# Kernel tuning notes

Measured on AMD Instinct MI355X. Metric: run time of the kernel, lower is better.

Reference implementation:

```python
import jax, jax.numpy as jnp
import numpy as np

C = 320        # in_channels == inner_dim (n_heads*d_head = 8*40)
HEADS = 8
DH = 40
CTX = 768
FF_INNER = 1280  # 4*C
G = 32         # GroupNorm groups


def _ln(x, w, b, eps=1e-5):
    m = x.mean(-1, keepdims=True)
    v = ((x - m) ** 2).mean(-1, keepdims=True)
    return (x - m) * jax.lax.rsqrt(v + eps) * w + b


def _attn(q, k, v, heads, scale):
    # faithful to source: split last dim as (d h) -> head index is fastest
    B, Lq, D = q.shape
    Lk = k.shape[1]
    dh = D // heads
    q = q.reshape(B, Lq, dh, heads).transpose(0, 3, 1, 2)  # b h i d
    k = k.reshape(B, Lk, dh, heads).transpose(0, 3, 1, 2)  # b h j d
    v = v.reshape(B, Lk, dh, heads).transpose(0, 3, 1, 2)
    sim = jnp.einsum('bhid,bhjd->bhij', q, k) * scale
    w = jax.nn.softmax(sim, axis=-1)
    o = jnp.einsum('bhij,bhjd->bhid', w, v)
    # merge as (h d): head index is slowest on output (matches source)
    return o.transpose(0, 2, 1, 3).reshape(B, Lq, heads * dh)


def setup_inputs() -> dict:
    key = jax.random.key(0)
    ks = jax.random.split(key, 20)
    n = lambda i, shape: jax.random.normal(ks[i], shape, jnp.float32) * 0.02
    z = lambda d: jnp.zeros((d,), jnp.float32)
    o = lambda d: jnp.ones((d,), jnp.float32)
    return dict(
        x=jax.random.normal(ks[0], (1, C, 64, 64), jnp.float32),
        context=jax.random.normal(ks[1], (1, 77, CTX), jnp.float32),
        gn_w=o(C), gn_b=z(C),
        w_in=n(2, (C, C)), b_in=z(C),
        ln1_w=o(C), ln1_b=z(C),
        wq1=n(3, (C, C)), wk1=n(4, (C, C)), wv1=n(5, (C, C)),
        wo1=n(6, (C, C)), bo1=z(C),
        ln2_w=o(C), ln2_b=z(C),
        wq2=n(7, (C, C)), wk2=n(8, (CTX, C)), wv2=n(9, (CTX, C)),
        wo2=n(10, (C, C)), bo2=z(C),
        ln3_w=o(C), ln3_b=z(C),
        wff1=n(11, (C, 2 * FF_INNER)), bff1=z(2 * FF_INNER),
        wff2=n(12, (FF_INNER, C)), bff2=z(C),
        w_out=n(13, (C, C)), b_out=z(C),
    )


def reference(x, context, gn_w, gn_b, w_in, b_in,
              ln1_w, ln1_b, wq1, wk1, wv1, wo1, bo1,
              ln2_w, ln2_b, wq2, wk2, wv2, wo2, bo2,
              ln3_w, ln3_b, wff1, bff1, wff2, bff2,
              w_out, b_out):
    B, Cc, H, W = x.shape
    scale = DH ** (-0.5)
    x_in = x
    # GroupNorm(32, eps=1e-6)
    g = x.reshape(B, G, Cc // G, H, W)
    m = g.mean((2, 3, 4), keepdims=True)
    v = ((g - m) ** 2).mean((2, 3, 4), keepdims=True)
    h = ((g - m) * jax.lax.rsqrt(v + 1e-6)).reshape(B, Cc, H, W)
    h = h * gn_w[None, :, None, None] + gn_b[None, :, None, None]
    # 1x1 conv in_proj
    h = jnp.einsum('bchw,co->bohw', h, w_in) + b_in[None, :, None, None]
    # b c h w -> b (h w) c
    t = h.transpose(0, 2, 3, 1).reshape(B, H * W, C)
    # --- transformer block (depth=1) ---
    # attn_1: self-attn; NOTE source applies k/v proj to the QUERY projection
    hn = _ln(t, ln1_w, ln1_b)
    q = hn @ wq1
    k = q @ wk1
    vv = q @ wv1
    t = t + (_attn(q, k, vv, HEADS, scale) @ wo1 + bo1)
    # attn_2: cross-attn with context
    hn = _ln(t, ln2_w, ln2_b)
    q = hn @ wq2
    k = context @ wk2
    vv = context @ wv2
    t = t + (_attn(q, k, vv, HEADS, scale) @ wo2 + bo2)
    # GEGLU feed-forward
    hn = _ln(t, ln3_w, ln3_b)
    p = hn @ wff1 + bff1
    a, gate = p[..., :FF_INNER], p[..., FF_INNER:]
    t = t + ((a * jax.nn.gelu(gate, approximate=False)) @ wff2 + bff2)
    # b (h w) c -> b c h w
    s = t.reshape(B, H, W, C).transpose(0, 3, 1, 2)
    out = jnp.einsum('bchw,co->bohw', s, w_out) + b_out[None, :, None, None]
    return out + x_in
```

## Files before the change

kernel.cpp:

```cpp
#include <hip/hip_runtime.h>
#include <hip/hip_bf16.h>
#include <math.h>

#define CCH 320
#define NHEADS 8
#define DH 40
#define HW 4096
#define FFI 1280

typedef __bf16 bf16x8 __attribute__((ext_vector_type(8)));
typedef unsigned short u16x8 __attribute__((ext_vector_type(8)));
typedef short s16x4 __attribute__((ext_vector_type(4)));
typedef float f32x4 __attribute__((ext_vector_type(4)));
typedef unsigned int u32x4 __attribute__((ext_vector_type(4)));

__device__ inline unsigned short f2bf(float f) {
    __hip_bfloat16 h = __float2bfloat16(f);
    return __builtin_bit_cast(unsigned short, h);
}
__device__ inline unsigned pk2bf(float a, float b) {
#if __has_builtin(__builtin_amdgcn_cvt_pk_bf16_f32)
    typedef __bf16 bf16x2 __attribute__((ext_vector_type(2)));
    bf16x2 r = __builtin_amdgcn_cvt_pk_bf16_f32(a, b);
    return __builtin_bit_cast(unsigned, r);
#else
    return (unsigned)f2bf(a) | ((unsigned)f2bf(b) << 16);
#endif
}
__device__ inline float bf2f(unsigned short u) {
    return __builtin_bit_cast(float, ((unsigned)u) << 16);
}
__device__ inline bf16x8 ldfrag(const unsigned short* p) {
    u16x8 raw = *reinterpret_cast<const u16x8*>(p);
    return __builtin_bit_cast(bf16x8, raw);
}
__device__ inline s16x4 pk2frag(unsigned a, unsigned b) {
    unsigned long long v = (unsigned long long)a | ((unsigned long long)b << 32);
    return __builtin_bit_cast(s16x4, v);
}

__global__ __launch_bounds__(256) void prep_w2(
    const float* __restrict__ w_in, const float* __restrict__ wq1,
    const float* __restrict__ wk1, const float* __restrict__ wv1,
    const float* __restrict__ wo1, const float* __restrict__ wq2,
    const float* __restrict__ wo2, const float* __restrict__ w_out,
    const float* __restrict__ wff1, const float* __restrict__ wff2,
    const float* __restrict__ wk2, const float* __restrict__ wv2,
    unsigned short* __restrict__ Wt) {
    __shared__ float tile[64][65];
    const int b = blockIdx.x, tid = threadIdx.x;
    const float* src;
    int K, stride, dstoff, k0, n0;
    bool glu = false;
    if (b < 200) {
        int m = b / 25, t = b % 25;
        k0 = (t / 5) * 64; n0 = (t % 5) * 64;
        K = 320; stride = 320; dstoff = m * 102400;
        src = (m == 0) ? w_in : (m == 1) ? wq1 : (m == 2) ? wk1 :
              (m == 3) ? wv1 : (m == 4) ? wo1 : (m == 5) ? wq2 :
              (m == 6) ? wo2 : w_out;
    } else if (b < 300) {
        int t = b - 200;
        k0 = (t / 5) * 64; n0 = (t % 5) * 64;
        K = 1280; stride = 320; dstoff = 1638400; src = wff2;
    } else if (b < 500) {
        int t = b - 300;
        k0 = (t / 40) * 64; n0 = (t % 40) * 64;
        K = 320; stride = 2560; dstoff = 819200; src = wff1; glu = true;
    } else if (b < 560) {
        int t = b - 500;
        k0 = (t / 5) * 64; n0 = (t % 5) * 64;
        K = 768; stride = 320; dstoff = 2048000; src = wk2;
    } else {
        int t = b - 560;
        k0 = (t / 5) * 64; n0 = (t % 5) * 64;
        K = 768; stride = 320; dstoff = 2048000 + 245760; src = wv2;
    }
#pragma unroll
    for (int i = 0; i < 16; ++i) {
        int idx = tid + i * 256;
        int r = idx >> 6, cn = idx & 63;
        int scol = glu ? ((n0 >> 1) + (cn >> 1) + (cn & 1) * FFI) : (n0 + cn);
        tile[r][cn] = src[(size_t)(k0 + r) * stride + scol];
    }
    __syncthreads();
#pragma unroll
    for (int i = 0; i < 16; ++i) {
        int idx = tid + i * 256;
        int cl = idx >> 6, cr = idx & 63;
        Wt[dstoff + (size_t)(n0 + cl) * K + k0 + cr] = f2bf(tile[cr][cl]);
    }
}

__global__ void pack_ctx(const float* __restrict__ ctx,
                         unsigned short* __restrict__ D) {
    int idx = blockIdx.x * 256 + threadIdx.x;
    int row = idx / 768, col = idx - row * 768;
    float v = (row < 77) ? ctx[row * 768 + col] : 0.f;
    D[idx] = f2bf(v);
}

__global__ __launch_bounds__(256) void gn_stats(const float* __restrict__ X,
                                                float2* __restrict__ part) {
    __shared__ float s1[256], s2[256];
    const int b = blockIdx.x, tid = threadIdx.x;
    const float* xg = X + b * 5120;
    float s = 0.f, sq = 0.f;
#pragma unroll
    for (int i = 0; i < 20; ++i) { float v = xg[tid + i * 256]; s += v; sq += v * v; }
    s1[tid] = s; s2[tid] = sq; __syncthreads();
    for (int off = 128; off > 0; off >>= 1) {
        if (tid < off) { s1[tid] += s1[tid + off]; s2[tid] += s2[tid + off]; }
        __syncthreads();
    }
    if (tid == 0) part[b] = make_float2(s1[0], s2[0]);
}

__global__ __launch_bounds__(256) void gn_apply(const float* __restrict__ X,
                                                const float2* __restrict__ part,
                                                const float* __restrict__ w,
                                                const float* __restrict__ b,
                                                unsigned short* __restrict__ Y) {
    __shared__ float tile[64][65];
    __shared__ float gm[32], gr[32];
    const int tid = threadIdx.x;
    const int hw0 = blockIdx.x * 64, c0 = blockIdx.y * 64;
    if (tid < 32) {
        float s = 0.f, sq = 0.f;
#pragma unroll
        for (int i = 0; i < 8; ++i) { float2 p = part[tid * 8 + i]; s += p.x; sq += p.y; }
        float mean = s * (1.f / 40960.f);
        float var  = sq * (1.f / 40960.f) - mean * mean;
        gm[tid] = mean; gr[tid] = rsqrtf(var + 1e-6f);
    }
#pragma unroll
    for (int i = 0; i < 16; ++i) {
        int idx = tid + i * 256;
        int r = idx >> 6, col = idx & 63;
        tile[r][col] = X[(size_t)(c0 + r) * HW + hw0 + col];
    }
    __syncthreads();
#pragma unroll
    for (int i = 0; i < 16; ++i) {
        int idx = tid + i * 256;
        int hwl = idx >> 6, cl = idx & 63;
        int c = c0 + cl, g = c / 10;
        float v = (tile[cl][hwl] - gm[g]) * gr[g] * w[c] + b[c];
        Y[(size_t)(hw0 + hwl) * CCH + c] = f2bf(v);
    }
}

__global__ __launch_bounds__(256) void ln_kernel(const float* __restrict__ X,
                                                 const float* __restrict__ w,
                                                 const float* __restrict__ b,
                                                 unsigned short* __restrict__ Y) {
    const int row  = blockIdx.x * 4 + (threadIdx.x >> 6);
    const int lane = threadIdx.x & 63;
    const float* xr = X + row * CCH;
    float v[5];
    float s = 0.f, sq = 0.f;
#pragma unroll
    for (int i = 0; i < 5; ++i) { v[i] = xr[lane + 64 * i]; s += v[i]; sq += v[i] * v[i]; }
#pragma unroll
    for (int off = 32; off > 0; off >>= 1) {
        s  += __shfl_xor(s, off, 64);
        sq += __shfl_xor(sq, off, 64);
    }
    const float mean = s * (1.f / 320.f);
    const float var  = sq * (1.f / 320.f) - mean * mean;
    const float rstd = rsqrtf(var + 1e-5f);
    unsigned short* yr = Y + row * CCH;
#pragma unroll
    for (int i = 0; i < 5; ++i) {
        int c = lane + 64 * i;
        yr[c] = f2bf((v[i] - mean) * rstd * w[c] + b[c]);
    }
}

template <int MT, int K>
__global__ __launch_bounds__(256) void gemm4(
    const unsigned short* __restrict__ A,
    const unsigned short* __restrict__ Bt,
    const float* __restrict__ bias,
    const float* __restrict__ res,
    void* __restrict__ Cout, void* __restrict__ Cout2,
    int N, int mode, float scale) {
    constexpr int NCH = K / 64;
    __shared__ __align__(16) unsigned short Ab[2][MT * 16 * 64];
    __shared__ __align__(16) unsigned short Bb[2][64 * 64];
    const int tid  = threadIdx.x;
    const int wave = tid >> 6, lane = tid & 63;
    const int quad = lane >> 4, c = lane & 15;
    const int m0 = blockIdx.y * (MT * 16);
    const int bn = blockIdx.x;

    f32x4 acc[MT];
#pragma unroll
    for (int i = 0; i < MT; ++i) acc[i] = (f32x4){0.f, 0.f, 0.f, 0.f};

    const unsigned short* aslab = A + (size_t)m0 * K;
    const unsigned short* bslab = Bt + (size_t)(bn * 64) * K;

    constexpr int ITA = MT * 16 * 8 / 256;
    int arow[ITA], aoff[ITA];
#pragma unroll
    for (int i = 0; i < ITA; ++i) {
        int idx = tid + i * 256;
        arow[i] = idx >> 3;
        int g = idx & 7;
        aoff[i] = arow[i] * 64 + ((g ^ (arow[i] & 7)) * 8);
    }
    int brow[2], boff[2];
#pragma unroll
    for (int i = 0; i < 2; ++i) {
        int idx = tid + i * 256;
        brow[i] = idx >> 3;
        int g = idx & 7;
        boff[i] = brow[i] * 64 + ((g ^ (brow[i] & 7)) * 8);
    }
    const int ag = (tid & 7) * 8;

    {
        u16x8 ra[ITA], rb[2];
#pragma unroll
        for (int i = 0; i < ITA; ++i)
            ra[i] = *(const u16x8*)(aslab + (size_t)arow[i] * K + ag);
#pragma unroll
        for (int i = 0; i < 2; ++i)
            rb[i] = *(const u16x8*)(bslab + (size_t)brow[i] * K + ag);
#pragma unroll
        for (int i = 0; i < ITA; ++i) *(u16x8*)&Ab[0][aoff[i]] = ra[i];
#pragma unroll
        for (int i = 0; i < 2; ++i) *(u16x8*)&Bb[0][boff[i]] = rb[i];
    }
    __syncthreads();

    const int swz0 = (quad ^ (c & 7)) * 8;
    const int swz1 = ((quad + 4) ^ (c & 7)) * 8;
#pragma unroll
    for (int ch = 0; ch < NCH; ++ch) {
        const int buf = ch & 1;
        u16x8 ra[ITA], rb[2];
        if (ch + 1 < NCH) {
            const int kb = (ch + 1) * 64;
#pragma unroll
            for (int i = 0; i < ITA; ++i)
                ra[i] = *(const u16x8*)(aslab + (size_t)arow[i] * K + kb + ag);
#pragma unroll
            for (int i = 0; i < 2; ++i)
                rb[i] = *(const u16x8*)(bslab + (size_t)brow[i] * K + kb + ag);
        }
        bf16x8 b0 = ldfrag(&Bb[buf][(wave * 16 + c) * 64 + swz0]);
        bf16x8 b1 = ldfrag(&Bb[buf][(wave * 16 + c) * 64 + swz1]);
#pragma unroll
        for (int mt = 0; mt < MT; ++mt) {
            bf16x8 a0 = ldfrag(&Ab[buf][(mt * 16 + c) * 64 + swz0]);
            bf16x8 a1 = ldfrag(&Ab[buf][(mt * 16 + c) * 64 + swz1]);
            acc[mt] = __builtin_amdgcn_mfma_f32_16x16x32_bf16(a0, b0, acc[mt], 0, 0, 0);
            acc[mt] = __builtin_amdgcn_mfma_f32_16x16x32_bf16(a1, b1, acc[mt], 0, 0, 0);
        }
        if (ch + 1 < NCH) {
            const int nb = buf ^ 1;
#pragma unroll
            for (int i = 0; i < ITA; ++i) *(u16x8*)&Ab[nb][aoff[i]] = ra[i];
#pragma unroll
            for (int i = 0; i < 2; ++i) *(u16x8*)&Bb[nb][boff[i]] = rb[i];
        }
        __syncthreads();
    }

    const int col = bn * 64 + wave * 16 + c;
    float bval = 0.f;
    if (bias) bval = (mode == 5) ? bias[(col >> 1) + (col & 1) * FFI] : bias[col];

    if (mode == 9) {
#pragma unroll
        for (int mt = 0; mt < MT; ++mt) {
            const int row0 = m0 + mt * 16 + quad * 4;
            float4 xv = *(const float4*)(res + (size_t)col * HW + row0);
            float4 ov;
            ov.x = acc[mt][0] + bval + xv.x;
            ov.y = acc[mt][1] + bval + xv.y;
            ov.z = acc[mt][2] + bval + xv.z;
            ov.w = acc[mt][3] + bval + xv.w;
            *(float4*)((float*)Cout + (size_t)col * HW + row0) = ov;
        }
        return;
    }
#pragma unroll
    for (int mt = 0; mt < MT; ++mt) {
#pragma unroll
        for (int r = 0; r < 4; ++r) {
            const int row = m0 + mt * 16 + quad * 4 + r;
            float v = acc[mt][r];
            if (mode == 0) {
                v += bval;
                if (res) v += res[(size_t)row * N + col];
                ((float*)Cout)[(size_t)row * N + col] = v;
            } else if (mode == 2) {
                int h = col & 7, d = col >> 3;
                ((unsigned short*)Cout)[(((size_t)h << 12) + row) * 64 + d] = f2bf(v * scale);
            } else if (mode == 4) {
                ((unsigned short*)Cout)[(size_t)row * N + col] =
                    f2bf(v + bval + res[(size_t)row * N + col]);
            } else if (mode == 5) {
                v += bval;
                float other = __shfl_xor(v, 1, 64);
                if ((c & 1) == 0) {
                    float g = 0.5f * other * (1.f + erff(other * 0.70710678118654752f));
                    ((unsigned short*)Cout)[(size_t)row * FFI + (col >> 1)] = f2bf(v * g);
                }
            } else if (mode == 6) {
                ((unsigned short*)Cout)[(size_t)row * N + col] = f2bf(v);
                int h = col & 7, d = col >> 3;
                ((unsigned short*)Cout2)[(((size_t)h << 12) + row) * 64 + d] = f2bf(v * scale);
            } else if (mode == 7) {
                if (col < 320) {
                    int h = col & 7, d = col >> 3;
                    ((unsigned short*)Cout)[(((size_t)h << 12) + row) * 64 + d] = f2bf(v);
                } else {
                    int c2 = col - 320;
                    int h = c2 & 7, d = c2 >> 3;
                    ((unsigned short*)Cout2)[(((size_t)(h * 48 + d)) << 12) + row] = f2bf(v);
                }
            } else {
                if (col < 320) {
                    int h = col & 7, d = col >> 3;
                    ((unsigned short*)Cout)[(((size_t)h << 7) + row) * 64 + d] = f2bf(v);
                } else {
                    int c2 = col - 320;
                    int h = c2 & 7, d = c2 >> 3;
                    ((unsigned short*)Cout2)[(size_t)(h * 48 + d) * 128 + row] = f2bf(v);
                }
            }
        }
    }
}

__global__ void set_ones(unsigned short* __restrict__ Vt,
                         unsigned short* __restrict__ Vc) {
    int idx = blockIdx.x * 256 + threadIdx.x;
    if (idx < 32768) {
        int h = idx >> 12, r = idx & 4095;
        Vt[((size_t)(h * 48 + 40) << 12) + r] = 0x3F80;
    } else {
        int j = idx - 32768;
        int h = j >> 7, r = j & 127;
        Vc[(h * 48 + 40) * 128 + r] = 0x3F80;
    }
}

template <int TILES, bool MASK>
__global__ __launch_bounds__(256) void attn8(
    const unsigned short* __restrict__ Qp,
    const unsigned short* __restrict__ Kp,
    const unsigned short* __restrict__ Vt,
    float* __restrict__ pO, float* __restrict__ pL,
    int Lk, int Lkp) {
    __shared__ __align__(16) unsigned short Kb[2][64 * 64];
    __shared__ __align__(16) unsigned short Vb[2][48 * 64];
    const int tid  = threadIdx.x;
    const int wave = tid >> 6, lane = tid & 63;
    const int quad = lane >> 4, c = lane & 15;
    const int id  = blockIdx.x;
    const int h   = id & 7;
    const int qt  = (id >> 3) & 31;
    const int seg = id >> 8;
    const int q0  = qt * 128 + wave * 32;

    const unsigned short* qbaseA = Qp + ((((size_t)h << 12) + q0 + c) << 6) + quad * 8;
    const bf16x8 bQA0 = ldfrag(qbaseA);
    const bf16x8 bQA1 = ldfrag(qbaseA + 32);
    const bf16x8 bQB0 = ldfrag(qbaseA + 1024);
    const bf16x8 bQB1 = ldfrag(qbaseA + 1024 + 32);

    f32x4 oA[3], oB[3];
#pragma unroll
    for (int i = 0; i < 3; ++i) {
        oA[i] = (f32x4){0.f, 0.f, 0.f, 0.f};
        oB[i] = (f32x4){0.f, 0.f, 0.f, 0.f};
    }

    const int kt0 = seg * TILES;
    const unsigned short* kglob = Kp + (((size_t)h * Lkp + kt0 * 64) << 6);
    const unsigned short* vglob = Vt + ((size_t)h * 48) * Lkp + kt0 * 64;

    const int r0 = lane >> 3;
    const int g  = lane & 7;
    int ldsoff[4];
    const unsigned short* gptr0[4];
#pragma unroll
    for (int i = 0; i < 4; ++i) {
        int s = wave + 4 * i;
        if (s < 8) {
            int row = s * 8 + r0;
            ldsoff[i] = row * 64 + (g ^ (row & 7)) * 8;
            gptr0[i]  = kglob + (size_t)row * 64 + g * 8;
        } else if (s < 14) {
            int d = (s - 8) * 8 + r0;
            ldsoff[i] = d * 64 + (g ^ (d & 7)) * 8;
            gptr0[i]  = vglob + (size_t)d * Lkp + g * 8;
        } else {
            ldsoff[i] = 0; gptr0[i] = nullptr;
        }
    }
    const bool isK[4] = {(wave + 0) < 8, (wave + 4) < 8, (wave + 8) < 8, (wave + 12) < 8};
    const bool act[4] = {true, true, true, (wave + 12) < 14};

    {
        u16x8 st[4];
#pragma unroll
        for (int i = 0; i < 4; ++i)
            if (act[i]) st[i] = *(const u16x8*)(gptr0[i]);
#pragma unroll
        for (int i = 0; i < 4; ++i)
            if (act[i]) {
                unsigned short* lp = isK[i] ? &Kb[0][ldsoff[i]] : &Vb[0][ldsoff[i]];
                *(u16x8*)lp = st[i];
            }
    }
    __syncthreads();

#pragma unroll
    for (int t = 0; t < TILES; ++t) {
        const int b = t & 1;
        u16x8 st[4];
        if (t + 1 < TILES) {
            const int kb = (t + 1) * 64;
#pragma unroll
            for (int i = 0; i < 4; ++i)
                if (act[i]) {
                    const unsigned short* gp =
                        isK[i] ? (gptr0[i] + (size_t)kb * 64) : (gptr0[i] + kb);
                    st[i] = *(const u16x8*)gp;
                }
        }
        const unsigned short* Kl = &Kb[b][0];
        const unsigned short* Vl = &Vb[b][0];
        const int sw0 = (quad ^ (c & 7)) * 8;
        const int sw1 = ((quad + 4) ^ (c & 7)) * 8;
        f32x4 sA[4], sB[4];
#pragma unroll
        for (int blk = 0; blk < 4; ++blk) {
            const int row = (blk * 16 + c) * 64;
            bf16x8 k0 = ldfrag(Kl + row + sw0);
            bf16x8 k1 = ldfrag(Kl + row + sw1);
            f32x4 zA = {0.f, 0.f, 0.f, 0.f};
            zA = __builtin_amdgcn_mfma_f32_16x16x32_bf16(k0, bQA0, zA, 0, 0, 0);
            zA = __builtin_amdgcn_mfma_f32_16x16x32_bf16(k1, bQA1, zA, 0, 0, 0);
            sA[blk] = zA;
            f32x4 zB = {0.f, 0.f, 0.f, 0.f};
            zB = __builtin_amdgcn_mfma_f32_16x16x32_bf16(k0, bQB0, zB, 0, 0, 0);
            zB = __builtin_amdgcn_mfma_f32_16x16x32_bf16(k1, bQB1, zB, 0, 0, 0);
            sB[blk] = zB;
        }
        if (MASK) {
            const int abs_kb = kt0 * 64 + t * 64;
#pragma unroll
            for (int blk = 0; blk < 4; ++blk)
#pragma unroll
                for (int r = 0; r < 4; ++r) {
                    bool inv = (abs_kb + blk * 16 + quad * 4 + r >= Lk);
                    sA[blk][r] = inv ? -30000.f : sA[blk][r];
                    sB[blk][r] = inv ? -30000.f : sB[blk][r];
                }
        }
        s16x4 PA[4], PB[4];
#pragma unroll
        for (int blk = 0; blk < 4; ++blk) {
            PA[blk] = pk2frag(pk2bf(exp2f(sA[blk][0]), exp2f(sA[blk][1])),
                              pk2bf(exp2f(sA[blk][2]), exp2f(sA[blk][3])));
            PB[blk] = pk2frag(pk2bf(exp2f(sB[blk][0]), exp2f(sB[blk][1])),
                              pk2bf(exp2f(sB[blk][2]), exp2f(sB[blk][3])));
        }
#pragma unroll
        for (int db = 0; db < 3; ++db) {
            const int dim = db * 16 + c;
            const unsigned short* vrow = Vl + dim * 64;
            const int dswz = dim & 7;
#pragma unroll
            for (int kb = 0; kb < 4; ++kb) {
                const int off = (((kb * 2 + (quad >> 1)) ^ dswz) * 8) + (quad & 1) * 4;
                s16x4 vf = *(const s16x4*)(vrow + off);
                oA[db] = __builtin_amdgcn_mfma_f32_16x16x16bf16_1k(vf, PA[kb], oA[db], 0, 0, 0);
                oB[db] = __builtin_amdgcn_mfma_f32_16x16x16bf16_1k(vf, PB[kb], oB[db], 0, 0, 0);
            }
        }
        if (t + 1 < TILES) {
            const int nb = b ^ 1;
#pragma unroll
            for (int i = 0; i < 4; ++i)
                if (act[i]) {
                    unsigned short* lp = isK[i] ? &Kb[nb][ldsoff[i]] : &Vb[nb][ldsoff[i]];
                    *(u16x8*)lp = st[i];
                }
        }
        __syncthreads();
    }
    const size_t base = ((size_t)(seg * 8 + h)) << 12;
    float* obA = pO + (base + q0 + c) * 40;
    *(float4*)(obA + quad * 4)      = make_float4(oA[0][0], oA[0][1], oA[0][2], oA[0][3]);
    *(float4*)(obA + 16 + quad * 4) = make_float4(oA[1][0], oA[1][1], oA[1][2], oA[1][3]);
    if (quad < 2)
        *(float4*)(obA + 32 + quad * 4) = make_float4(oA[2][0], oA[2][1], oA[2][2], oA[2][3]);
    float* obB = pO + (base + q0 + 16 + c) * 40;
    *(float4*)(obB + quad * 4)      = make_float4(oB[0][0], oB[0][1], oB[0][2], oB[0][3]);
    *(float4*)(obB + 16 + quad * 4) = make_float4(oB[1][0], oB[1][1], oB[1][2], oB[1][3]);
    if (quad < 2)
        *(float4*)(obB + 32 + quad * 4) = make_float4(oB[2][0], oB[2][1], oB[2][2], oB[2][3]);
    if (quad == 2) {
        pL[base + q0 + c]      = oA[2][0];
        pL[base + q0 + 16 + c] = oB[2][0];
    }
}

__global__ __launch_bounds__(256) void attn_combine2(
    const float* __restrict__ pO, const float* __restrict__ pL,
    unsigned short* __restrict__ O, int S) {
    int idx = blockIdx.x * 256 + threadIdx.x;
    int h = idx / (HW * 10);
    int rem = idx - h * (HW * 10);
    int row = rem / 10, dg = rem - row * 10;
    float4 num = make_float4(0.f, 0.f, 0.f, 0.f);
    float den = 0.f;
    for (int s = 0; s < S; ++s) {
        size_t base = ((size_t)(s * 8 + h)) << 12;
        float4 p = *(const float4*)(pO + (base + row) * 40 + dg * 4);
        num.x += p.x; num.y += p.y; num.z += p.z; num.w += p.w;
        den += pL[base + row];
    }
    float inv = 1.f / den;
    unsigned short* ob = O + (size_t)row * CCH + h * DH + dg * 4;
    unsigned lo = pk2bf(num.x * inv, num.y * inv);
    unsigned hi = pk2bf(num.z * inv, num.w * inv);
    *(uint2*)ob = make_uint2(lo, hi);
}

extern "C" void kernel_launch(void* const* d_in, const int* in_sizes, int n_in,
                              void* d_out, int out_size, void* d_ws, size_t ws_size,
                              hipStream_t stream) {
    const float* x     = (const float*)d_in[0];
    const float* ctx   = (const float*)d_in[1];
    const float* gn_w  = (const float*)d_in[2];
    const float* gn_b  = (const float*)d_in[3];
    const float* w_in  = (const float*)d_in[4];
    const float* b_in  = (const float*)d_in[5];
    const float* ln1_w = (const float*)d_in[6];
    const float* ln1_b = (const float*)d_in[7];
    const float* wq1   = (const float*)d_in[8];
    const float* wk1   = (const float*)d_in[9];
    const float* wv1   = (const float*)d_in[10];
    const float* wo1   = (const float*)d_in[11];
    const float* bo1   = (const float*)d_in[12];
    const float* ln2_w = (const float*)d_in[13];
    const float* ln2_b = (const float*)d_in[14];
    const float* wq2   = (const float*)d_in[15];
    const float* wk2   = (const float*)d_in[16];
    const float* wv2   = (const float*)d_in[17];
    const float* wo2   = (const float*)d_in[18];
    const float* bo2   = (const float*)d_in[19];
    const float* ln3_w = (const float*)d_in[20];
    const float* ln3_b = (const float*)d_in[21];
    const float* wff1  = (const float*)d_in[22];
    const float* bff1  = (const float*)d_in[23];
    const float* wff2  = (const float*)d_in[24];
    const float* bff2  = (const float*)d_in[25];
    const float* w_out = (const float*)d_in[26];
    const float* b_out = (const float*)d_in[27];
    float* out = (float*)d_out;

    const int NT = HW * CCH;
    float* ws = (float*)d_ws;
    float* t_   = ws;
    float* y_   = t_ + NT;
    float* pO   = y_ + NT;
    float* pL   = pO + 4 * 8 * 4096 * 40;
    float2* gnp = (float2*)(pL + 4 * 8 * 4096);
    unsigned short* u = (unsigned short*)(gnp + 256);
    unsigned short* a_bf = u;                  u += NT;
    unsigned short* q_bf = u;                  u += NT;
    unsigned short* o_bf = u;                  u += NT;
    unsigned short* t_bf = u;                  u += NT;
    unsigned short* g_bf = u;                  u += HW * FFI;
    unsigned short* Qp   = u;                  u += 8 * 4096 * 64;
    unsigned short* Kp   = u;                  u += 8 * 4096 * 64;
    unsigned short* Vt   = u;                  u += 8 * 48 * 4096;
    unsigned short* Kc   = u;                  u += 8 * 128 * 64;
    unsigned short* Vc   = u;                  u += 8 * 48 * 128;
    unsigned short* Wt   = u;                  u += 2048000 + 2 * 245760;
    unsigned short* ctx_bf = u;                u += 128 * 768;

    const unsigned short* w_inT  = Wt;
    const unsigned short* wq1T   = Wt + 102400;
    const unsigned short* wk1T   = Wt + 204800;
    const unsigned short* wo1T   = Wt + 409600;
    const unsigned short* wq2T   = Wt + 512000;
    const unsigned short* wo2T   = Wt + 614400;
    const unsigned short* w_outT = Wt + 716800;
    const unsigned short* wff1T  = Wt + 819200;
    const unsigned short* wff2T  = Wt + 1638400;
    const unsigned short* wk2T   = Wt + 2048000;

    const float qscale = 0.15811388300841897f * 1.4426950408889634f;

    prep_w2<<<620, 256, 0, stream>>>(w_in, wq1, wk1, wv1, wo1, wq2, wo2, w_out,
                                     wff1, wff2, wk2, wv2, Wt);
    hipMemsetAsync(Qp, 0,
                   (size_t)(8 * 4096 * 64 * 2 + 8 * 48 * 4096 + 8 * 128 * 64 + 8 * 48 * 128) * 2,
                   stream);
    set_ones<<<132, 256, 0, stream>>>(Vt, Vc);
    pack_ctx<<<384, 256, 0, stream>>>(ctx, ctx_bf);

    gn_stats<<<256, 256, 0, stream>>>(x, gnp);
    gn_apply<<<dim3(64, 5), 256, 0, stream>>>(x, gnp, gn_w, gn_b, a_bf);
    gemm4<2, 320><<<dim3(5, 128), 256, 0, stream>>>(a_bf, w_inT, b_in, nullptr, t_, nullptr, CCH, 0, 1.f);
    ln_kernel<<<1024, 256, 0, stream>>>(t_, ln1_w, ln1_b, a_bf);
    gemm4<2, 320><<<dim3(5, 128), 256, 0, stream>>>(a_bf, wq1T, nullptr, nullptr, q_bf, Qp, CCH, 6, qscale);
    gemm4<2, 320><<<dim3(10, 128), 256, 0, stream>>>(q_bf, wk1T, nullptr, nullptr, Kp, Vt, 640, 7, 1.f);
    attn8<16, false><<<1024, 256, 0, stream>>>(Qp, Kp, Vt, pO, pL, HW, HW);
    attn_combine2<<<1280, 256, 0, stream>>>(pO, pL, o_bf, 4);
    gemm4<2, 320><<<dim3(5, 128), 256, 0, stream>>>(o_bf, wo1T, bo1, t_, t_, nullptr, CCH, 0, 1.f);
    ln_kernel<<<1024, 256, 0, stream>>>(t_, ln2_w, ln2_b, a_bf);
    gemm4<2, 320><<<dim3(5, 128), 256, 0, stream>>>(a_bf, wq2T, nullptr, nullptr, Qp, nullptr, CCH, 2, qscale);
    gemm4<2, 768><<<dim3(10, 4), 256, 0, stream>>>(ctx_bf, wk2T, nullptr, nullptr, Kc, Vc, 640, 8, 1.f);
    attn8<2, true><<<256, 256, 0, stream>>>(Qp, Kc, Vc, pO, pL, 77, 128);
    attn_combine2<<<1280, 256, 0, stream>>>(pO, pL, o_bf, 1);
    gemm4<2, 320><<<dim3(5, 128), 256, 0, stream>>>(o_bf, wo2T, bo2, t_, t_, nullptr, CCH, 0, 1.f);
    ln_kernel<<<1024, 256, 0, stream>>>(t_, ln3_w, ln3_b, a_bf);
    gemm4<2, 320><<<dim3(40, 128), 256, 0, stream>>>(a_bf, wff1T, bff1, nullptr, g_bf, nullptr, 2 * FFI, 5, 1.f);
    gemm4<2, 1280><<<dim3(5, 128), 256, 0, stream>>>(g_bf, wff2T, bff2, t_, t_bf, nullptr, CCH, 4, 1.f);
    gemm4<2, 320><<<dim3(5, 128), 256, 0, stream>>>(t_bf, w_outT, b_out, x, out, nullptr, CCH, 9, 1.f);
}
```

Baseline: 313.2 us.

## Use fast exp2/rcp intrinsics, polynomial GELU, and MFMA priority hints

Replaces erff-based GELU in the GEGLU epilogue with an Abramowitz-Stegun polynomial that uses hardware rcp and exp2. Switches softmax exp2f to the raw amdgcn exp2 intrinsic and the combine division to a hardware reciprocal. Wraps the attention MFMA loops in s_setprio to favour matrix issue across waves. These cut transcendental instruction cost at a small accuracy loss, since the erf approximation carries roughly 1e-7 absolute error.

```diff
diff --git a/kernel.cpp b/kernel.cpp
--- a/kernel.cpp
+++ b/kernel.cpp
@@ -37,6 +37,32 @@
 __device__ inline s16x4 pk2frag(unsigned a, unsigned b) {
     unsigned long long v = (unsigned long long)a | ((unsigned long long)b << 32);
     return __builtin_bit_cast(s16x4, v);
+}
+
+__device__ inline float ex2(float x) {
+#if __has_builtin(__builtin_amdgcn_exp2f)
+    return __builtin_amdgcn_exp2f(x);
+#else
+    return exp2f(x);
+#endif
+}
+__device__ inline float fast_rcp(float x) {
+#if __has_builtin(__builtin_amdgcn_rcpf)
+    return __builtin_amdgcn_rcpf(x);
+#else
+    return 1.f / x;
+#endif
+}
+__device__ inline float fast_gelu(float x) {
+    float z = fabsf(x) * 0.70710678118654752f;
+    float t = fast_rcp(fmaf(0.3275911f, z, 1.f));
+    float poly = fmaf(fmaf(fmaf(fmaf(1.061405429f, t, -1.453152027f), t,
+                               1.421413741f), t, -0.284496736f), t,
+                      0.254829592f) * t;
+    float e = ex2(z * z * -1.4426950408889634f);
+    float erfz = 1.f - poly * e;
+    float s = copysignf(erfz, x);
+    return 0.5f * x * (1.f + s);
 }
 
 __global__ __launch_bounds__(256) void prep_w2(
@@ -307,7 +333,7 @@
                 v += bval;
                 float other = __shfl_xor(v, 1, 64);
                 if ((c & 1) == 0) {
-                    float g = 0.5f * other * (1.f + erff(other * 0.70710678118654752f));
+                    float g = fast_gelu(other);
                     ((unsigned short*)Cout)[(size_t)row * FFI + (col >> 1)] = f2bf(v * g);
                 }
             } else if (mode == 6) {
@@ -440,6 +466,7 @@
         const int sw0 = (quad ^ (c & 7)) * 8;
         const int sw1 = ((quad + 4) ^ (c & 7)) * 8;
         f32x4 sA[4], sB[4];
+        __builtin_amdgcn_s_setprio(1);
 #pragma unroll
         for (int blk = 0; blk < 4; ++blk) {
             const int row = (blk * 16 + c) * 64;
@@ -454,6 +481,7 @@
             zB = __builtin_amdgcn_mfma_f32_16x16x32_bf16(k1, bQB1, zB, 0, 0, 0);
             sB[blk] = zB;
         }
+        __builtin_amdgcn_s_setprio(0);
         if (MASK) {
             const int abs_kb = kt0 * 64 + t * 64;
 #pragma unroll
@@ -468,11 +496,12 @@
         s16x4 PA[4], PB[4];
 #pragma unroll
         for (int blk = 0; blk < 4; ++blk) {
-            PA[blk] = pk2frag(pk2bf(exp2f(sA[blk][0]), exp2f(sA[blk][1])),
-                              pk2bf(exp2f(sA[blk][2]), exp2f(sA[blk][3])));
-            PB[blk] = pk2frag(pk2bf(exp2f(sB[blk][0]), exp2f(sB[blk][1])),
-                              pk2bf(exp2f(sB[blk][2]), exp2f(sB[blk][3])));
-        }
+            PA[blk] = pk2frag(pk2bf(ex2(sA[blk][0]), ex2(sA[blk][1])),
+                              pk2bf(ex2(sA[blk][2]), ex2(sA[blk][3])));
+            PB[blk] = pk2frag(pk2bf(ex2(sB[blk][0]), ex2(sB[blk][1])),
+                              pk2bf(ex2(sB[blk][2]), ex2(sB[blk][3])));
+        }
+        __builtin_amdgcn_s_setprio(1);
 #pragma unroll
         for (int db = 0; db < 3; ++db) {
             const int dim = db * 16 + c;
@@ -486,6 +515,7 @@
                 oB[db] = __builtin_amdgcn_mfma_f32_16x16x16bf16_1k(vf, PB[kb], oB[db], 0, 0, 0);
             }
         }
+        __builtin_amdgcn_s_setprio(0);
         if (t + 1 < TILES) {
             const int nb = b ^ 1;
 #pragma unroll
@@ -529,7 +559,7 @@
         num.x += p.x; num.y += p.y; num.z += p.z; num.w += p.w;
         den += pL[base + row];
     }
-    float inv = 1.f / den;
+    float inv = fast_rcp(den);
     unsigned short* ob = O + (size_t)row * CCH + h * DH + dg * 4;
     unsigned lo = pk2bf(num.x * inv, num.y * inv);
     unsigned hi = pk2bf(num.z * inv, num.w * inv);
```

After: 300.3 us. -4.1%, faster.
